# Kernel tuning notes

Hardware: AMD Instinct MI355X
Metric: run time of the kernel (lower is better)

Reference implementation:

```python
import jax, jax.numpy as jnp
import numpy as np

D = 2048   # input_dim == output_dim (original scatter-adds into zeros_like(x))
E = 16     # num_experts
K = 2      # expert_top_k
B = 2048   # tokens


def setup_inputs() -> dict:
    key = jax.random.key(0)
    ks = jax.random.split(key, 6)
    s = 0.02
    return {
        "x":  jax.random.normal(ks[0], (B, D), jnp.float32),
        "W1": (jax.random.normal(ks[1], (E, D, D), jnp.float32) * s),
        "b1": jnp.zeros((E, D), jnp.float32),
        "W2": (jax.random.normal(ks[2], (E, D, D), jnp.float32) * s),
        "b2": jnp.zeros((E, D), jnp.float32),
        "Wg": (jax.random.normal(ks[3], (D, E), jnp.float32) * s),
        "bg": jnp.zeros((E,), jnp.float32),
    }


def reference(x, W1, b1, W2, b2, Wg, bg):
    # --- gating ---
    gate_scores = x @ Wg + bg                                  # (B, E)
    topk_scores, topk_idx = jax.lax.top_k(gate_scores, K)      # (B, K)
    gate_act = jax.nn.softmax(topk_scores, axis=-1)            # (B, K) softmax over top-k only
    onehot = jax.nn.one_hot(topk_idx, E, dtype=x.dtype)        # (B, K, E)
    combine = jnp.einsum('bk,bke->be', gate_act, onehot)       # (B, E) gate weight per expert (0 if unrouted)
    routing_mask = onehot.sum(axis=1)                          # (B, E) in {0,1}

    # --- expert MLPs (dense grouped form; unrouted tokens zeroed by combine) ---
    h = jax.nn.relu(jnp.einsum('bd,edh->ebh', x, W1) + b1[:, None, :])   # (E, B, D)
    y = jnp.einsum('ebh,eho->ebo', h, W2) + b2[:, None, :]               # (E, B, D)
    out = jnp.einsum('ebo,be->bo', y, combine)                           # (B, D) weighted scatter-add combine

    # --- aux losses (torch.var is unbiased, ddof=1) ---
    loads = routing_mask.sum(axis=0)                            # tokens per expert
    load_loss = jnp.var(loads, ddof=1) / (E * (B / E))          # balance_factor = num_experts * expected_load = B
    imp = jax.nn.softmax(gate_scores, axis=-1).sum(axis=0)      # (E,)
    importance_loss = jnp.var(imp, ddof=1) / (imp.mean() + 1e-8)
    return out, load_loss, importance_loss
```

## Files before the change

kernel.cpp:

```cpp
#include <hip/hip_runtime.h>
#include <hip/hip_bf16.h>
#include <stdint.h>

#define DIM   2048
#define NEXP  16
#define TOPK  2
#define NTOK  2048
#define NSLOT (NTOK*TOPK)

typedef __bf16 bf16_t;
typedef __attribute__((ext_vector_type(4))) __bf16 bf16x4;
typedef __attribute__((ext_vector_type(8))) __bf16 bf16x8;
typedef __attribute__((ext_vector_type(4))) float f32x4;

#define WS_COUNTS    1024
#define WS_OFFS      1152
#define WS_TOK_TOP   4096
#define WS_TOK_GATE  20480
#define WS_SLOT_TOK  36864
#define WS_SLOT_GATE 53248
#define WS_IMPP      69632
#define WS_XBF       262144
#define WS_H         (WS_XBF + NTOK*DIM*2)

__global__ __launch_bounds__(256) void k_gate(const float* __restrict__ x,
                                              const float* __restrict__ Wg,
                                              const float* __restrict__ bg,
                                              float* __restrict__ imp_partial,
                                              int* __restrict__ tok_top,
                                              float* __restrict__ tok_gate,
                                              bf16_t* __restrict__ xb) {
    const int tok  = blockIdx.x * 4 + (threadIdx.x >> 6);
    const int lane = threadIdx.x & 63;
    const float* xr = x + (size_t)tok * DIM;
    bf16_t* xbr = xb + (size_t)tok * DIM;

    float acc[NEXP];
#pragma unroll
    for (int e = 0; e < NEXP; e++) acc[e] = 0.f;

#pragma unroll
    for (int i = 0; i < 8; i++) {
        int d = (i * 64 + lane) * 4;
        float4 xv = *reinterpret_cast<const float4*>(xr + d);
        bf16x4 o;
        o[0] = (bf16_t)xv.x; o[1] = (bf16_t)xv.y; o[2] = (bf16_t)xv.z; o[3] = (bf16_t)xv.w;
        *reinterpret_cast<bf16x4*>(xbr + d) = o;
        const float4* wr = reinterpret_cast<const float4*>(Wg + (size_t)d * NEXP);
#pragma unroll
        for (int c = 0; c < 4; c++) {
            float xc = (&xv.x)[c];
#pragma unroll
            for (int j = 0; j < 4; j++) {
                float4 w = wr[c * 4 + j];
                acc[j * 4 + 0] += xc * w.x;
                acc[j * 4 + 1] += xc * w.y;
                acc[j * 4 + 2] += xc * w.z;
                acc[j * 4 + 3] += xc * w.w;
            }
        }
    }
#pragma unroll
    for (int e = 0; e < NEXP; e++) {
#pragma unroll
        for (int off = 32; off > 0; off >>= 1) acc[e] += __shfl_xor(acc[e], off, 64);
    }

    if (lane == 0) {
        float sc[NEXP];
#pragma unroll
        for (int e = 0; e < NEXP; e++) sc[e] = acc[e] + bg[e];
        float mx = sc[0];
#pragma unroll
        for (int e = 1; e < NEXP; e++) mx = fmaxf(mx, sc[e]);
        float p[NEXP], sum = 0.f;
#pragma unroll
        for (int e = 0; e < NEXP; e++) { p[e] = expf(sc[e] - mx); sum += p[e]; }
        float inv = 1.f / sum;
#pragma unroll
        for (int e = 0; e < NEXP; e++) imp_partial[tok * NEXP + e] = p[e] * inv;
        int i0 = 0;
#pragma unroll
        for (int e = 1; e < NEXP; e++) if (sc[e] > sc[i0]) i0 = e;
        int i1 = -1;
#pragma unroll
        for (int e = 0; e < NEXP; e++)
            if (e != i0 && (i1 < 0 || sc[e] > sc[i1])) i1 = e;
        float g0 = 1.f / (1.f + expf(sc[i1] - sc[i0]));
        tok_top[tok * 2 + 0] = i0; tok_top[tok * 2 + 1] = i1;
        tok_gate[tok * 2 + 0] = g0; tok_gate[tok * 2 + 1] = 1.f - g0;
    }
}

__global__ __launch_bounds__(256) void k_finalize(const float* __restrict__ imp_partial,
                                                  const int* __restrict__ tok_top,
                                                  const float* __restrict__ tok_gate,
                                                  int* __restrict__ counts,
                                                  int* __restrict__ offs,
                                                  int* __restrict__ slot_tok,
                                                  float* __restrict__ slot_gate,
                                                  float* __restrict__ losses) {
    __shared__ int   scnt[NEXP];
    __shared__ int   soff[NEXP];
    __shared__ int   scur[NEXP];
    __shared__ float ired[16][NEXP + 1];
    const int t = threadIdx.x;
    if (t < NEXP) { scnt[t] = 0; scur[t] = 0; }
    __syncthreads();
    for (int i = t; i < NSLOT; i += 256) atomicAdd(&scnt[tok_top[i]], 1);
    {
        const int e = t & 15, ch = t >> 4;
        float s = 0.f;
        for (int r = ch * 128; r < ch * 128 + 128; r++) s += imp_partial[r * NEXP + e];
        ired[ch][e] = s;
    }
    __syncthreads();
    if (t == 0) {
        int o = 0;
        float cntf[NEXP];
        for (int e = 0; e < NEXP; e++) {
            counts[e] = scnt[e]; soff[e] = o; offs[e] = o; o += scnt[e]; cntf[e] = (float)scnt[e];
        }
        offs[NEXP] = o;
        float m = (float)o / NEXP, v = 0.f;
        for (int e = 0; e < NEXP; e++) { float d = cntf[e] - m; v += d * d; }
        losses[0] = (v / (NEXP - 1)) / (float)NTOK;
        float imp[NEXP];
        for (int e = 0; e < NEXP; e++) {
            float s = 0.f;
            for (int ch = 0; ch < 16; ch++) s += ired[ch][e];
            imp[e] = s;
        }
        float ms = 0.f;
        for (int e = 0; e < NEXP; e++) ms += imp[e];
        ms /= NEXP;
        float vv = 0.f;
        for (int e = 0; e < NEXP; e++) { float d = imp[e] - ms; vv += d * d; }
        losses[1] = (vv / (NEXP - 1)) / (ms + 1e-8f);
    }
    __syncthreads();
    for (int i = t; i < NSLOT; i += 256) {
        int e = tok_top[i];
        int pos = atomicAdd(&scur[e], 1);
        int slot = soff[e] + pos;
        slot_tok[slot] = i >> 1;
        slot_gate[slot] = tok_gate[i];
    }
}

#define BM 256
#define BN 64
#define BK 32
#define NSTEPS (DIM/BK)
#define APITCH 32
#define BPITCH 40

template <int PHASE>
__global__ __launch_bounds__(512, 6) void k_gemm(const float* __restrict__ Wall,
                                                 const float* __restrict__ bias,
                                                 const bf16_t* __restrict__ Asrc,
                                                 const int* __restrict__ counts,
                                                 const int* __restrict__ offs,
                                                 const int* __restrict__ slot_tok,
                                                 const float* __restrict__ slot_gate,
                                                 bf16_t* __restrict__ Hout,
                                                 float* __restrict__ out) {
    const int e  = blockIdx.z;
    const int n0 = blockIdx.x * BN;
    const int m0 = blockIdx.y * BM;
    const int cnt = counts[e];
    if (m0 >= cnt) return;
    const int off = offs[e];

    __shared__ bf16_t As[2][BM * APITCH];
    __shared__ bf16_t Bs[2][BN * BPITCH];

    const int tid  = threadIdx.x;
    const int lane = tid & 63, wv = tid >> 6;
    const int wm = wv & 3, wn = wv >> 2;
    const int l15 = lane & 15, q = lane >> 4;

    const bf16_t* arow[2];
#pragma unroll
    for (int i = 0; i < 2; i++) {
        int rl = wv * 32 + i * 16 + (lane >> 2);
        int slot = off + m0 + rl;
        slot = slot < (NSLOT - 1) ? slot : (NSLOT - 1);
        int srow = (PHASE == 1) ? slot_tok[slot] : slot;
        int gchunk = (lane & 3) ^ ((lane >> 3) & 3);
        arow[i] = Asrc + (size_t)srow * DIM + gchunk * 8;
    }
    const int bn = tid & 63, kh = tid >> 6;
    const float* bsrc = Wall + (size_t)e * DIM * DIM + (size_t)(kh * 4) * DIM + n0 + bn;
    bf16_t* bdst0 = &Bs[0][bn * BPITCH + kh * 4];
    bf16_t* bdst1 = &Bs[1][bn * BPITCH + kh * 4];

    f32x4 acc[4][2] = {};
    float bv[4];

#pragma unroll
    for (int i = 0; i < 2; i++) {
        bf16_t* ldst = &As[0][(wv * 32 + i * 16) * APITCH];
        __builtin_amdgcn_global_load_lds(
            (const __attribute__((address_space(1))) uint32_t*)(arow[i]),
            (__attribute__((address_space(3))) uint32_t*)ldst, 16, 0, 0);
    }
#pragma unroll
    for (int kk = 0; kk < 4; kk++) bv[kk] = bsrc[(size_t)kk * DIM];
    {
        bf16x4 pk;
#pragma unroll
        for (int kk = 0; kk < 4; kk++) pk[kk] = (bf16_t)bv[kk];
        *reinterpret_cast<bf16x4*>(bdst0) = pk;
    }
    __syncthreads();

    const int akey = (l15 >> 1) & 3;

    for (int t = 0; t < NSTEPS; t++) {
        const int cur = t & 1;
        const int k1 = (t + 1) * BK;
        if (t + 1 < NSTEPS) {
#pragma unroll
            for (int i = 0; i < 2; i++) {
                bf16_t* ldst = &As[cur ^ 1][(wv * 32 + i * 16) * APITCH];
                __builtin_amdgcn_global_load_lds(
                    (const __attribute__((address_space(1))) uint32_t*)(arow[i] + k1),
                    (__attribute__((address_space(3))) uint32_t*)ldst, 16, 0, 0);
            }
            const float* bs = bsrc + (size_t)k1 * DIM;
#pragma unroll
            for (int kk = 0; kk < 4; kk++) bv[kk] = bs[(size_t)kk * DIM];
        }
        bf16x8 af[4], bfr[2];
#pragma unroll
        for (int mf = 0; mf < 4; mf++)
            af[mf] = *reinterpret_cast<const bf16x8*>(
                &As[cur][(wm * 64 + mf * 16 + l15) * APITCH + ((q ^ akey) * 8)]);
#pragma unroll
        for (int nf = 0; nf < 2; nf++)
            bfr[nf] = *reinterpret_cast<const bf16x8*>(
                &Bs[cur][(wn * 32 + nf * 16 + l15) * BPITCH + q * 8]);
#pragma unroll
        for (int mf = 0; mf < 4; mf++)
#pragma unroll
            for (int nf = 0; nf < 2; nf++)
                acc[mf][nf] = __builtin_amdgcn_mfma_f32_16x16x32_bf16(af[mf], bfr[nf], acc[mf][nf], 0, 0, 0);
        if (t + 1 < NSTEPS) {
            bf16x4 pk;
#pragma unroll
            for (int kk = 0; kk < 4; kk++) pk[kk] = (bf16_t)bv[kk];
            *reinterpret_cast<bf16x4*>((cur ^ 1) ? bdst1 : bdst0) = pk;
        }
        __syncthreads();
    }

    const int rows_here = cnt - m0;
#pragma unroll
    for (int mf = 0; mf < 4; mf++) {
#pragma unroll
        for (int r = 0; r < 4; r++) {
            int rl = wm * 64 + mf * 16 + q * 4 + r;
            if (rl >= rows_here) continue;
            int slot = off + m0 + rl;
            if (PHASE == 1) {
#pragma unroll
                for (int nf = 0; nf < 2; nf++) {
                    int col = n0 + wn * 32 + nf * 16 + l15;
                    float h = acc[mf][nf][r] + bias[e * DIM + col];
                    h = fmaxf(h, 0.f);
                    Hout[(size_t)slot * DIM + col] = (bf16_t)h;
                }
            } else {
                float g = slot_gate[slot];
                int tok = slot_tok[slot];
#pragma unroll
                for (int nf = 0; nf < 2; nf++) {
                    int col = n0 + wn * 32 + nf * 16 + l15;
                    float y = acc[mf][nf][r] + bias[e * DIM + col];
                    atomicAdd(&out[(size_t)tok * DIM + col], g * y);
                }
            }
        }
    }
}

extern "C" void kernel_launch(void* const* d_in, const int* in_sizes, int n_in,
                              void* d_out, int out_size, void* d_ws, size_t ws_size,
                              hipStream_t stream) {
    const float* x  = (const float*)d_in[0];
    const float* W1 = (const float*)d_in[1];
    const float* b1 = (const float*)d_in[2];
    const float* W2 = (const float*)d_in[3];
    const float* b2 = (const float*)d_in[4];
    const float* Wg = (const float*)d_in[5];
    const float* bg = (const float*)d_in[6];
    float* out = (float*)d_out;
    char*  ws  = (char*)d_ws;

    int*    counts    = (int*)(ws + WS_COUNTS);
    int*    offs      = (int*)(ws + WS_OFFS);
    int*    tok_top   = (int*)(ws + WS_TOK_TOP);
    float*  tok_gate  = (float*)(ws + WS_TOK_GATE);
    int*    slot_tok  = (int*)(ws + WS_SLOT_TOK);
    float*  slot_gate = (float*)(ws + WS_SLOT_GATE);
    float*  imp_part  = (float*)(ws + WS_IMPP);
    bf16_t* xbf       = (bf16_t*)(ws + WS_XBF);
    bf16_t* H         = (bf16_t*)(ws + WS_H);

    hipMemsetAsync(out, 0, (size_t)NTOK * DIM * sizeof(float), stream);

    k_gate<<<NTOK / 4, 256, 0, stream>>>(x, Wg, bg, imp_part, tok_top, tok_gate, xbf);
    k_finalize<<<1, 256, 0, stream>>>(imp_part, tok_top, tok_gate, counts, offs,
                                      slot_tok, slot_gate, out + (size_t)NTOK * DIM);

    dim3 grid(DIM / BN, NTOK / BM, NEXP);
    k_gemm<1><<<grid, 512, 0, stream>>>(W1, b1, xbf, counts, offs, slot_tok, slot_gate, H, nullptr);
    k_gemm<2><<<grid, 512, 0, stream>>>(W2, b2, H, counts, offs, slot_tok, slot_gate, nullptr, out);
}
```

Baseline: 877.7 us.

## Deepen grouped-GEMM pipeline with triple-buffered A tiles and two-step prefetch

Restructures the expert GEMM main loop so A tiles are triple-buffered in LDS and B weights are prefetched two K-steps ahead into two alternating register sets. Hand-placed vmcnt waits, raw s_barrier and sched_barrier replace __syncthreads, and MFMA blocks are wrapped in s_setprio to favour the math wave. The goal is to hide global load latency behind more in-flight memory traffic. Launch bounds drop from 6 to 4 blocks per CU to leave room for the extra LDS and registers, which lowers occupancy. The fixed vmcnt(6) waits may not fence the final tiles in the tail iterations, where fewer loads are outstanding.

```diff
diff --git a/kernel.cpp b/kernel.cpp
--- a/kernel.cpp
+++ b/kernel.cpp
@@ -155,8 +155,51 @@
 #define APITCH 32
 #define BPITCH 40
 
+#define AISSUE(kidx, abuf)                                                          \
+    _Pragma("unroll")                                                               \
+    for (int i_ = 0; i_ < 2; i_++) {                                                \
+        bf16_t* ldst_ = &(abuf)[(wv * 32 + i_ * 16) * APITCH];                      \
+        __builtin_amdgcn_global_load_lds(                                           \
+            (const __attribute__((address_space(1))) uint32_t*)(arow[i_] + (kidx) * BK), \
+            (__attribute__((address_space(3))) uint32_t*)ldst_, 16, 0, 0);          \
+    }
+
+#define BLOAD(kidx, bv)                                                             \
+    { const float* bs_ = bsrc + (size_t)((kidx) * BK) * DIM;                        \
+      _Pragma("unroll")                                                             \
+      for (int kk_ = 0; kk_ < 4; kk_++) (bv)[kk_] = bs_[(size_t)kk_ * DIM]; }
+
+#define BWRITE(bv, bbuf)                                                            \
+    { bf16x4 pk_;                                                                   \
+      _Pragma("unroll")                                                             \
+      for (int kk_ = 0; kk_ < 4; kk_++) pk_[kk_] = (bf16_t)(bv)[kk_];               \
+      *reinterpret_cast<bf16x4*>(&(bbuf)[bn * BPITCH + kh * 4]) = pk_; }
+
+#define COMPUTE(abuf, bbuf)                                                         \
+    { bf16x8 af_[4], bf_[2];                                                        \
+      _Pragma("unroll")                                                             \
+      for (int mf_ = 0; mf_ < 4; mf_++)                                             \
+          af_[mf_] = *reinterpret_cast<const bf16x8*>(                              \
+              &(abuf)[(wm * 64 + mf_ * 16 + l15) * APITCH + ((q ^ akey) * 8)]);     \
+      _Pragma("unroll")                                                             \
+      for (int nf_ = 0; nf_ < 2; nf_++)                                             \
+          bf_[nf_] = *reinterpret_cast<const bf16x8*>(                              \
+              &(bbuf)[(wn * 32 + nf_ * 16 + l15) * BPITCH + q * 8]);                \
+      __builtin_amdgcn_s_setprio(1);                                                \
+      _Pragma("unroll")                                                             \
+      for (int mf_ = 0; mf_ < 4; mf_++)                                             \
+          _Pragma("unroll")                                                         \
+          for (int nf_ = 0; nf_ < 2; nf_++)                                         \
+              acc[mf_][nf_] = __builtin_amdgcn_mfma_f32_16x16x32_bf16(af_[mf_], bf_[nf_], acc[mf_][nf_], 0, 0, 0); \
+      __builtin_amdgcn_s_setprio(0); }
+
+#define ENDBAR()                                                                    \
+    asm volatile("s_waitcnt lgkmcnt(0)" ::: "memory");                              \
+    __builtin_amdgcn_s_barrier();                                                   \
+    __builtin_amdgcn_sched_barrier(0);
+
 template <int PHASE>
-__global__ __launch_bounds__(512, 6) void k_gemm(const float* __restrict__ Wall,
+__global__ __launch_bounds__(512, 4) void k_gemm(const float* __restrict__ Wall,
                                                  const float* __restrict__ bias,
                                                  const bf16_t* __restrict__ Asrc,
                                                  const int* __restrict__ counts,
@@ -172,7 +215,7 @@
     if (m0 >= cnt) return;
     const int off = offs[e];
 
-    __shared__ bf16_t As[2][BM * APITCH];
+    __shared__ bf16_t As[3][BM * APITCH];
     __shared__ bf16_t Bs[2][BN * BPITCH];
 
     const int tid  = threadIdx.x;
@@ -192,67 +235,39 @@
     }
     const int bn = tid & 63, kh = tid >> 6;
     const float* bsrc = Wall + (size_t)e * DIM * DIM + (size_t)(kh * 4) * DIM + n0 + bn;
-    bf16_t* bdst0 = &Bs[0][bn * BPITCH + kh * 4];
-    bf16_t* bdst1 = &Bs[1][bn * BPITCH + kh * 4];
+
+    const int akey = (l15 >> 1) & 3;
 
     f32x4 acc[4][2] = {};
-    float bv[4];
-
-#pragma unroll
-    for (int i = 0; i < 2; i++) {
-        bf16_t* ldst = &As[0][(wv * 32 + i * 16) * APITCH];
-        __builtin_amdgcn_global_load_lds(
-            (const __attribute__((address_space(1))) uint32_t*)(arow[i]),
-            (__attribute__((address_space(3))) uint32_t*)ldst, 16, 0, 0);
-    }
-#pragma unroll
-    for (int kk = 0; kk < 4; kk++) bv[kk] = bsrc[(size_t)kk * DIM];
-    {
-        bf16x4 pk;
-#pragma unroll
-        for (int kk = 0; kk < 4; kk++) pk[kk] = (bf16_t)bv[kk];
-        *reinterpret_cast<bf16x4*>(bdst0) = pk;
-    }
-    __syncthreads();
-
-    const int akey = (l15 >> 1) & 3;
-
-    for (int t = 0; t < NSTEPS; t++) {
-        const int cur = t & 1;
-        const int k1 = (t + 1) * BK;
-        if (t + 1 < NSTEPS) {
-#pragma unroll
-            for (int i = 0; i < 2; i++) {
-                bf16_t* ldst = &As[cur ^ 1][(wv * 32 + i * 16) * APITCH];
-                __builtin_amdgcn_global_load_lds(
-                    (const __attribute__((address_space(1))) uint32_t*)(arow[i] + k1),
-                    (__attribute__((address_space(3))) uint32_t*)ldst, 16, 0, 0);
-            }
-            const float* bs = bsrc + (size_t)k1 * DIM;
-#pragma unroll
-            for (int kk = 0; kk < 4; kk++) bv[kk] = bs[(size_t)kk * DIM];
-        }
-        bf16x8 af[4], bfr[2];
-#pragma unroll
-        for (int mf = 0; mf < 4; mf++)
-            af[mf] = *reinterpret_cast<const bf16x8*>(
-                &As[cur][(wm * 64 + mf * 16 + l15) * APITCH + ((q ^ akey) * 8)]);
-#pragma unroll
-        for (int nf = 0; nf < 2; nf++)
-            bfr[nf] = *reinterpret_cast<const bf16x8*>(
-                &Bs[cur][(wn * 32 + nf * 16 + l15) * BPITCH + q * 8]);
-#pragma unroll
-        for (int mf = 0; mf < 4; mf++)
-#pragma unroll
-            for (int nf = 0; nf < 2; nf++)
-                acc[mf][nf] = __builtin_amdgcn_mfma_f32_16x16x32_bf16(af[mf], bfr[nf], acc[mf][nf], 0, 0, 0);
-        if (t + 1 < NSTEPS) {
-            bf16x4 pk;
-#pragma unroll
-            for (int kk = 0; kk < 4; kk++) pk[kk] = (bf16_t)bv[kk];
-            *reinterpret_cast<bf16x4*>((cur ^ 1) ? bdst1 : bdst0) = pk;
-        }
-        __syncthreads();
+    float bvA[4], bvB[4];
+
+    bf16_t* Ac = As[0];
+    bf16_t* An = As[1];
+    bf16_t* Af = As[2];
+
+    AISSUE(0, Ac);
+    BLOAD(0, bvA);
+    __builtin_amdgcn_sched_barrier(0);
+    AISSUE(1, An);
+    BLOAD(1, bvB);
+    asm volatile("s_waitcnt vmcnt(6)" ::: "memory");
+    BWRITE(bvA, Bs[0]);
+    ENDBAR();
+
+    for (int t = 0; t < NSTEPS; t += 2) {
+        if (t + 2 < NSTEPS) { AISSUE(t + 2, Af); BLOAD(t + 2, bvA); }
+        COMPUTE(Ac, Bs[0]);
+        asm volatile("s_waitcnt vmcnt(6)" ::: "memory");
+        if (t + 1 < NSTEPS) BWRITE(bvB, Bs[1]);
+        ENDBAR();
+        { bf16_t* tmp = Ac; Ac = An; An = Af; Af = tmp; }
+
+        if (t + 3 < NSTEPS) { AISSUE(t + 3, Af); BLOAD(t + 3, bvB); }
+        COMPUTE(Ac, Bs[1]);
+        asm volatile("s_waitcnt vmcnt(6)" ::: "memory");
+        if (t + 2 < NSTEPS) BWRITE(bvA, Bs[0]);
+        ENDBAR();
+        { bf16_t* tmp = Ac; Ac = An; An = Af; Af = tmp; }
     }
 
     const int rows_here = cnt - m0;
```

After: 825.4 us. 6.0% less time.
